# Kernel tuning notes

Measured on AMD Instinct MI355X. Metric: run time of the kernel, lower is better.

Reference implementation:

```python
import jax, jax.numpy as jnp
import numpy as np

N = 100_000   # nodes
E = 1_600_000 # edges
V = 100_000   # vocab
G = 256       # graphs in batch
D = 64        # emb/hidden dim


def setup_inputs() -> dict:
    key = jax.random.key(0)
    ks = jax.random.split(key, 12)
    x_tokens = jax.random.randint(ks[0], (N, 1), 0, V)
    edge_index = jax.random.randint(ks[1], (2, E), 0, N)
    batch = jnp.sort(jax.random.randint(ks[2], (N,), 0, G))
    s = 0.02
    return {
        "x_tokens": x_tokens,
        "edge_index": edge_index,
        "batch": batch,
        "emb_table": jax.random.normal(ks[3], (V, D), jnp.float32) * s,
        "W0": jax.random.normal(ks[4], (D, D), jnp.float32) * s,
        "b0": jnp.zeros((D,), jnp.float32),
        "W1": jax.random.normal(ks[5], (D, D), jnp.float32) * s,
        "b1": jnp.zeros((D,), jnp.float32),
        "W2": jax.random.normal(ks[6], (D, D), jnp.float32) * s,
        "b2": jnp.zeros((D,), jnp.float32),
        "Wc1": jax.random.normal(ks[7], (2 * D, D), jnp.float32) * s,
        "bc1": jnp.zeros((D,), jnp.float32),
        "Wc2": jax.random.normal(ks[8], (D, 2), jnp.float32) * s,
        "bc2": jnp.zeros((2,), jnp.float32),
    }


def _gcn_norm(edge_index, n_nodes):
    # add self loops, compute symmetric normalization coefficients
    loop = jnp.arange(n_nodes, dtype=edge_index.dtype)
    src = jnp.concatenate([edge_index[0], loop])
    dst = jnp.concatenate([edge_index[1], loop])
    deg = jax.ops.segment_sum(jnp.ones_like(dst, jnp.float32), dst, num_segments=n_nodes)
    dinv = jnp.where(deg > 0, deg ** -0.5, 0.0)
    norm = dinv[src] * dinv[dst]  # [E+N]
    return src, dst, norm


def _gcn_conv(x, W, b, src, dst, norm, n_nodes):
    x = x @ W                                   # [N, D]
    msg = x[src] * norm[:, None]                # gather + scale, [E+N, D]
    out = jax.ops.segment_sum(msg, dst, num_segments=n_nodes)
    return out + b


def reference(x_tokens, edge_index, batch, emb_table, W0, b0, W1, b1, W2, b2, Wc1, bc1, Wc2, bc2):
    n = x_tokens.shape[0]
    src, dst, norm = _gcn_norm(edge_index, n)
    x = emb_table[x_tokens[:, 0]]               # [N, D]
    for W, b in ((W0, b0), (W1, b1), (W2, b2)):
        x = jax.nn.relu(_gcn_conv(x, W, b, src, dst, norm, n))
    # dual pooling over graph ids
    cnt = jax.ops.segment_sum(jnp.ones((n,), x.dtype), batch, num_segments=G)
    h_sum = jax.ops.segment_sum(x, batch, num_segments=G)
    h_mean = h_sum / jnp.maximum(cnt, 1.0)[:, None]
    h_max = jax.ops.segment_max(x, batch, num_segments=G)
    h_max = jnp.where(jnp.isfinite(h_max), h_max, 0.0)
    h = jnp.concatenate([h_mean, h_max], axis=-1)   # [G, 2D]
    logits = jax.nn.relu(h @ Wc1 + bc1) @ Wc2 + bc2  # [G, 2]
    return logits
```

## Files before the change

### kernel.cpp

```cpp
#include <hip/hip_runtime.h>
#include <hip/hip_fp16.h>
#include <math.h>


#define BKT_LOG 9
#define BKT (1 << BKT_LOG)
#define CHUNK 4096

typedef _Float16 h2 __attribute__((ext_vector_type(2)));
typedef _Float16 f16x8 __attribute__((ext_vector_type(8)));
typedef float f32x4 __attribute__((ext_vector_type(4)));

union HU { unsigned u; h2 h; };
__device__ inline h2 h2bits(unsigned u) { HU x; x.u = u; return x.h; }

#if __has_builtin(__builtin_amdgcn_fdot2)
#define FDOT2(a, b, c) __builtin_amdgcn_fdot2((a), (b), (c), false)
#else
__device__ inline float FDOT2(h2 a, h2 b, float c) {
  return (float)a.x * (float)b.x + (float)a.y * (float)b.y + c;
}
#endif

#define MASK_X 0x00003C00u
#define MASK_Y 0x3C000000u

__device__ inline void acc8c(const uint4& v, float* acc) {
  const unsigned* w = (const unsigned*)&v;
#pragma unroll
  for (int k = 0; k < 4; k++) {
    h2 hv = h2bits(w[k]);
    acc[2 * k]     = FDOT2(hv, h2bits(MASK_X), acc[2 * k]);
    acc[2 * k + 1] = FDOT2(hv, h2bits(MASK_Y), acc[2 * k + 1]);
  }
}

__global__ __launch_bounds__(256) void k_wcvt(const float* __restrict__ W0,
                                              const float* __restrict__ W1,
                                              const float* __restrict__ W2,
                                              _Float16* __restrict__ Wf,
                                              int* __restrict__ gcur,
                                              float* __restrict__ hz, int hzn) {
  if (blockIdx.x < 3) {
    const float* W = (blockIdx.x == 0) ? W0 : (blockIdx.x == 1) ? W1 : W2;
    _Float16* out = Wf + blockIdx.x * 4096;
    for (int i = threadIdx.x; i < 4096; i += 256) {
      int c = i >> 10, s = (i >> 9) & 1, l = (i >> 3) & 63, j = i & 7;
      int k = 32 * s + 8 * (l >> 4) + j;
      int ncol = 16 * c + (l & 15);
      out[i] = (_Float16)W[k * 64 + ncol];
    }
  } else if (blockIdx.x == 3) {
    gcur[threadIdx.x] = 0;
  } else {
    for (int i = threadIdx.x; i < hzn; i += 256) hz[i] = 0.f;
  }
}

__global__ __launch_bounds__(256) void k_part(const int* __restrict__ src,
                                              const int* __restrict__ dst,
                                              int* __restrict__ gcur,
                                              int* __restrict__ ebuf,
                                              int E, int S) {
  __shared__ int sA[CHUNK];
  __shared__ int dA[CHUNK];
  __shared__ int h[256], base[256];
  int tid = threadIdx.x;
  long c0 = (long)blockIdx.x * CHUNK;
  int m = (int)min((long)CHUNK, (long)E - c0);
  h[tid] = 0;
  __syncthreads();
  for (int i = tid; i < m; i += 256) {
    int s = src[c0 + i];
    int d = dst[c0 + i];
    sA[i] = s;
    dA[i] = d;
    atomicAdd(&h[d >> BKT_LOG], 1);
  }
  __syncthreads();
  if (h[tid]) base[tid] = atomicAdd(&gcur[tid], h[tid]);
  __syncthreads();
  h[tid] = 0;
  __syncthreads();
  for (int i = tid; i < m; i += 256) {
    int s = sA[i], d = dA[i];
    int k = d >> BKT_LOG;
    int p = base[k] + atomicAdd(&h[k], 1);
    if (p < S)
      ebuf[k * S + p] = ((d & (BKT - 1)) << 17) | s;
  }
}

__global__ __launch_bounds__(512) void k_bplace(const int* __restrict__ ebuf,
                                                const int* __restrict__ gcur,
                                                int* __restrict__ off,
                                                int* __restrict__ eend,
                                                int* __restrict__ csrc,
                                                float* __restrict__ dinv,
                                                int N, int S) {
  __shared__ int s[512];
  __shared__ int cur[512];
  int b = blockIdx.x, tid = threadIdx.x;
  int n0 = b << BKT_LOG;
  int nn = min(BKT, N - n0);
  int e0 = b * S;
  int cnt = min(gcur[b], S);
  s[tid] = 0;
  __syncthreads();
  for (int e = tid; e < cnt; e += 512) atomicAdd(&s[ebuf[e0 + e] >> 17], 1);
  __syncthreads();
  int deg = s[tid];
  for (int d = 1; d < 512; d <<= 1) {
    int t = (tid >= d) ? s[tid - d] : 0;
    __syncthreads();
    s[tid] += t;
    __syncthreads();
  }
  int excl = s[tid] - deg;
  if (tid < nn) {
    off[n0 + tid] = e0 + excl;
    eend[n0 + tid] = e0 + excl + deg;
    dinv[n0 + tid] = 1.0f / sqrtf((float)(1 + deg));
  }
  cur[tid] = excl;
  __syncthreads();
  for (int e = tid; e < cnt; e += 512) {
    int p = ebuf[e0 + e];
    int pos = e0 + atomicAdd(&cur[p >> 17], 1);
    csrc[pos] = p & 0x1FFFF;
  }
}

template <bool EMB>
__global__ __launch_bounds__(256) void k_mfmamm(const _Float16* __restrict__ y,
                                                const int* __restrict__ tok,
                                                const float* __restrict__ emb,
                                                const _Float16* __restrict__ Wf,
                                                const float* __restrict__ dinv,
                                                float scale,
                                                _Float16* __restrict__ xh,
                                                int n, int npad) {
  __shared__ _Float16 lds[4 * 16 * 72];
  int w = threadIdx.x >> 6, l = threadIdx.x & 63;
  int m = l & 15, q = l >> 4;
  int rbase = blockIdx.x * 64 + w * 16;

  f16x8 a0, a1;
  if (EMB) {
    int node = min(rbase + m, n - 1);
    const float* er = emb + (size_t)tok[node] * 64;
    float4 v0 = *(const float4*)(er + q * 8);
    float4 v1 = *(const float4*)(er + q * 8 + 4);
    float4 v2 = *(const float4*)(er + 32 + q * 8);
    float4 v3 = *(const float4*)(er + 32 + q * 8 + 4);
    a0[0] = (_Float16)v0.x; a0[1] = (_Float16)v0.y; a0[2] = (_Float16)v0.z; a0[3] = (_Float16)v0.w;
    a0[4] = (_Float16)v1.x; a0[5] = (_Float16)v1.y; a0[6] = (_Float16)v1.z; a0[7] = (_Float16)v1.w;
    a1[0] = (_Float16)v2.x; a1[1] = (_Float16)v2.y; a1[2] = (_Float16)v2.z; a1[3] = (_Float16)v2.w;
    a1[4] = (_Float16)v3.x; a1[5] = (_Float16)v3.y; a1[6] = (_Float16)v3.z; a1[7] = (_Float16)v3.w;
  } else {
    int node = rbase + m;
    a0 = *(const f16x8*)(y + ((size_t)(q >> 1) * npad + node) * 16 + (q & 1) * 8);
    a1 = *(const f16x8*)(y + ((size_t)((q >> 1) + 2) * npad + node) * 16 + (q & 1) * 8);
  }
  float4 d4 = *(const float4*)(dinv + rbase + q * 4);

  const f16x8* wf = (const f16x8*)Wf + l;
  f32x4 acc[4];
#pragma unroll
  for (int c = 0; c < 4; c++) {
    f32x4 z = {0.f, 0.f, 0.f, 0.f};
    z = __builtin_amdgcn_mfma_f32_16x16x32_f16(a0, wf[(c * 2 + 0) * 64], z, 0, 0, 0);
    z = __builtin_amdgcn_mfma_f32_16x16x32_f16(a1, wf[(c * 2 + 1) * 64], z, 0, 0, 0);
    acc[c] = z;
  }

  const float ds[4] = {d4.x * scale, d4.y * scale, d4.z * scale, d4.w * scale};
  _Float16* ldw = lds + w * 16 * 72;
#pragma unroll
  for (int c = 0; c < 4; c++)
#pragma unroll
    for (int r = 0; r < 4; r++)
      ldw[(q * 4 + r) * 72 + c * 16 + m] = (_Float16)(acc[c][r] * ds[r]);
  __syncthreads();

  int row2 = l & 15, c2 = l >> 4;
  int node = rbase + row2;
  if (node < n) {
    const uint4* s4 = (const uint4*)(ldw + row2 * 72 + c2 * 16);
    uint4 v0 = s4[0], v1 = s4[1];
    uint4* dst = (uint4*)(xh + ((size_t)c2 * npad + node) * 16);
    dst[0] = v0;
    dst[1] = v1;
  }
}

__global__ __launch_bounds__(256) void k_aggregate(const int* __restrict__ off,
                                                   const int* __restrict__ eend,
                                                   const int* __restrict__ csrc,
                                                   const float* __restrict__ dinv,
                                                   const _Float16* __restrict__ xh,
                                                   const float* __restrict__ bias,
                                                   _Float16* __restrict__ outp,
                                                   int n, int npad) {
  int c = blockIdx.x & 3;
  int lane = threadIdx.x & 63;
  int n4 = lane >> 4, g = (lane >> 1) & 7, o = lane & 1;
  int t = (blockIdx.x >> 2) * 16 + (threadIdx.x >> 6) * 4 + n4;
  bool valid = t < n;
  int tc = valid ? t : n - 1;
  int e0 = off[tc], e1 = eend[tc];
  if (!valid) e1 = e0;
  const uint4* x4 = (const uint4*)xh + (size_t)c * npad * 2;

  float acc[8];
#pragma unroll
  for (int k = 0; k < 8; k++) acc[k] = 0.f;
  if (g == 0) acc8c(x4[(size_t)tc * 2 + o], acc);

  int iA = e0 + g;
  bool aA = iA < e1, aB = iA + 8 < e1;
  int sA = aA ? csrc[iA] : 0;
  int sB = aB ? csrc[iA + 8] : 0;
  while (aA) {
    uint4 vA = x4[(size_t)sA * 2 + o];
    uint4 vB;
    if (aB) vB = x4[(size_t)sB * 2 + o];
    int iN = iA + 16;
    bool aN = iN < e1, aM = iN + 8 < e1;
    int sN = 0, sM = 0;
    if (aN) sN = csrc[iN];
    if (aM) sM = csrc[iN + 8];
    acc8c(vA, acc);
    if (aB) acc8c(vB, acc);
    iA = iN; aA = aN; sA = sN;
    aB = aM; sB = sM;
  }

#pragma unroll
  for (int mm = 2; mm <= 8; mm <<= 1) {
#pragma unroll
    for (int k = 0; k < 8; k++) acc[k] += __shfl_xor(acc[k], mm);
  }

  if (valid && g == 0) {
    float sc = dinv[t] * (1.0f / 256.0f);
    int f0 = c * 16 + o * 8;
    float4 bb0 = *(const float4*)(bias + f0);
    float4 bb1 = *(const float4*)(bias + f0 + 4);
    const float bs[8] = {bb0.x, bb0.y, bb0.z, bb0.w, bb1.x, bb1.y, bb1.z, bb1.w};
    _Float16 hh[8];
#pragma unroll
    for (int k = 0; k < 8; k++)
      hh[k] = (_Float16)(fmaxf(acc[k] * sc + bs[k], 0.f) * 4096.f);
    *(uint4*)(outp + ((size_t)c * npad + t) * 16 + o * 8) = *(const uint4*)hh;
  }
}

__global__ __launch_bounds__(256) void k_pool(const _Float16* __restrict__ x,
                                              const int* __restrict__ batch,
                                              float* __restrict__ hsum,
                                              float* __restrict__ hmax,
                                              int* __restrict__ cntg,
                                              int n, int npad) {
  int wid = (blockIdx.x * blockDim.x + threadIdx.x) >> 6;
  int lane = threadIdx.x & 63;
  int i0 = wid * 64;
  if (i0 >= n) return;
  int i1 = min(i0 + 64, n);
  size_t sb = (size_t)(lane >> 4) * npad * 16 + (lane & 15);
  int batch_l = (i0 + lane < n) ? batch[i0 + lane] : 0;
  float gsum = 0.f, gmax = 0.f;
  int cur = __shfl(batch_l, 0);
  int c = 0;
  for (int i = i0; i < i1; i++) {
    int g = __shfl(batch_l, i - i0);
    if (g != cur) {
      atomicAdd(&hsum[cur * 64 + lane], gsum);
      atomicMax((int*)&hmax[cur * 64 + lane], __float_as_int(gmax));
      if (lane == 0) atomicAdd(&cntg[cur], c);
      gsum = 0.f; gmax = 0.f; c = 0; cur = g;
    }
    float v = (float)x[sb + (size_t)i * 16];
    gsum += v;
    gmax = fmaxf(gmax, v);
    c++;
  }
  atomicAdd(&hsum[cur * 64 + lane], gsum);
  atomicMax((int*)&hmax[cur * 64 + lane], __float_as_int(gmax));
  if (lane == 0) atomicAdd(&cntg[cur], c);
}

__global__ __launch_bounds__(64) void k_cls(const float* __restrict__ hsum,
                                            const float* __restrict__ hmax,
                                            const int* __restrict__ cnt,
                                            const float* __restrict__ Wc1,
                                            const float* __restrict__ bc1,
                                            const float* __restrict__ Wc2,
                                            const float* __restrict__ bc2,
                                            float* __restrict__ out) {
  __shared__ float h[128];
  __shared__ float hid[64];
  int g = blockIdx.x, j = threadIdx.x;
  int c = cnt[g];
  float cf = (float)(c > 0 ? c : 1);
  h[j] = hsum[g * 64 + j] / cf * (1.0f / 4096.0f);
  h[64 + j] = hmax[g * 64 + j] * (1.0f / 4096.0f);
  __syncthreads();
  float acc = bc1[j];
  for (int k = 0; k < 128; k++) acc += h[k] * Wc1[k * 64 + j];
  hid[j] = fmaxf(acc, 0.f);
  __syncthreads();
  if (j < 2) {
    float a = bc2[j];
    for (int k = 0; k < 64; k++) a += hid[k] * Wc2[k * 2 + j];
    out[g * 2 + j] = a;
  }
}

extern "C" void kernel_launch(void* const* d_in, const int* in_sizes, int n_in,
                              void* d_out, int out_size, void* d_ws, size_t ws_size,
                              hipStream_t stream) {
  const int N = in_sizes[0];
  const int E = in_sizes[1] / 2;
  const int G = out_size / 2;
  const int B = (N + BKT - 1) >> BKT_LOG;
  const int Npad = (N + 63) & ~63;
  const int S = ((((E + B - 1) / B) * 3 / 2 + 256) + 3) & ~3;

  const int* tok   = (const int*)d_in[0];
  const int* ei    = (const int*)d_in[1];
  const int* batch = (const int*)d_in[2];
  const float* emb = (const float*)d_in[3];
  const float* W0 = (const float*)d_in[4];  const float* b0 = (const float*)d_in[5];
  const float* W1 = (const float*)d_in[6];  const float* b1 = (const float*)d_in[7];
  const float* W2 = (const float*)d_in[8];  const float* b2 = (const float*)d_in[9];
  const float* Wc1 = (const float*)d_in[10]; const float* bc1 = (const float*)d_in[11];
  const float* Wc2 = (const float*)d_in[12]; const float* bc2 = (const float*)d_in[13];
  const int* srcp = ei;
  const int* dstp = ei + E;

  int* off    = (int*)d_ws;
  int* eend   = off + N;
  float* dinv = (float*)(eend + N);
  int* gcur   = (int*)(dinv + Npad);
  _Float16* Wf = (_Float16*)(gcur + 256);
  int* csrc   = (int*)(Wf + 3 * 4096);
  _Float16* xh = (_Float16*)(csrc + (size_t)B * S);
  _Float16* y  = xh + (size_t)Npad * 64;
  int* ebuf   = (int*)y;
  float* hsum = (float*)(y + (size_t)Npad * 64);
  float* hmax = hsum + (size_t)G * 64;
  int*   cntg = (int*)(hmax + (size_t)G * 64);

  auto cdiv = [](long a, long b) { return (int)((a + b - 1) / b); };
  const int aggBlocks = 4 * cdiv(N, 16);

  k_wcvt<<<5, 256, 0, stream>>>(W0, W1, W2, Wf, gcur, hsum, G * 129);

  k_part<<<cdiv(E, CHUNK), 256, 0, stream>>>(srcp, dstp, gcur, ebuf, E, S);
  k_bplace<<<B, 512, 0, stream>>>(ebuf, gcur, off, eend, csrc, dinv, N, S);

  k_mfmamm<true><<<cdiv(N, 64), 256, 0, stream>>>(nullptr, tok, emb, Wf, dinv, 256.f, xh, N, Npad);
  k_aggregate<<<aggBlocks, 256, 0, stream>>>(off, eend, csrc, dinv, xh, b0, y, N, Npad);

  k_mfmamm<false><<<cdiv(N, 64), 256, 0, stream>>>(y, nullptr, nullptr, Wf + 4096, dinv, 1.f / 16.f, xh, N, Npad);
  k_aggregate<<<aggBlocks, 256, 0, stream>>>(off, eend, csrc, dinv, xh, b1, y, N, Npad);

  k_mfmamm<false><<<cdiv(N, 64), 256, 0, stream>>>(y, nullptr, nullptr, Wf + 8192, dinv, 1.f / 16.f, xh, N, Npad);
  k_aggregate<<<aggBlocks, 256, 0, stream>>>(off, eend, csrc, dinv, xh, b2, y, N, Npad);

  k_pool<<<cdiv(N, 256), 256, 0, stream>>>(y, batch, hsum, hmax, cntg, N, Npad);

  k_cls<<<G, 64, 0, stream>>>(hsum, hmax, cntg, Wc1, bc1, Wc2, bc2, (float*)d_out);
}
```

Measured before the change: 333.5 us.

## Switch node features to row-major layout and use one wave per node in aggregation

Node feature buffers change from a four-chunk column-blocked layout (16 features per chunk, padded by Npad) to a plain row-major layout of 64 fp16 values per node. The aggregation kernel is rewritten so one wave handles one destination node, with each lane accumulating one feature in fp32 over neighbours read in groups of four. This replaces the earlier scheme where each wave split edges across lane groups with 16-byte loads per lane, fdot2 accumulation and a cross-lane shuffle reduction. Each edge now costs a 128-byte coalesced row read, but the per-lane loads are only 2 bytes and the loop over edges runs serially within a wave, which may lower memory-level parallelism.

```diff
diff --git a/kernel.cpp b/kernel.cpp
--- a/kernel.cpp
+++ b/kernel.cpp
@@ -10,30 +10,6 @@
 typedef _Float16 h2 __attribute__((ext_vector_type(2)));
 typedef _Float16 f16x8 __attribute__((ext_vector_type(8)));
 typedef float f32x4 __attribute__((ext_vector_type(4)));
-
-union HU { unsigned u; h2 h; };
-__device__ inline h2 h2bits(unsigned u) { HU x; x.u = u; return x.h; }
-
-#if __has_builtin(__builtin_amdgcn_fdot2)
-#define FDOT2(a, b, c) __builtin_amdgcn_fdot2((a), (b), (c), false)
-#else
-__device__ inline float FDOT2(h2 a, h2 b, float c) {
-  return (float)a.x * (float)b.x + (float)a.y * (float)b.y + c;
-}
-#endif
-
-#define MASK_X 0x00003C00u
-#define MASK_Y 0x3C000000u
-
-__device__ inline void acc8c(const uint4& v, float* acc) {
-  const unsigned* w = (const unsigned*)&v;
-#pragma unroll
-  for (int k = 0; k < 4; k++) {
-    h2 hv = h2bits(w[k]);
-    acc[2 * k]     = FDOT2(hv, h2bits(MASK_X), acc[2 * k]);
-    acc[2 * k + 1] = FDOT2(hv, h2bits(MASK_Y), acc[2 * k + 1]);
-  }
-}
 
 __global__ __launch_bounds__(256) void k_wcvt(const float* __restrict__ W0,
                                               const float* __restrict__ W1,
@@ -139,7 +115,7 @@
                                                 const float* __restrict__ dinv,
                                                 float scale,
                                                 _Float16* __restrict__ xh,
-                                                int n, int npad) {
+                                                int n) {
   __shared__ _Float16 lds[4 * 16 * 72];
   int w = threadIdx.x >> 6, l = threadIdx.x & 63;
   int m = l & 15, q = l >> 4;
@@ -159,8 +135,9 @@
     a1[4] = (_Float16)v3.x; a1[5] = (_Float16)v3.y; a1[6] = (_Float16)v3.z; a1[7] = (_Float16)v3.w;
   } else {
     int node = rbase + m;
-    a0 = *(const f16x8*)(y + ((size_t)(q >> 1) * npad + node) * 16 + (q & 1) * 8);
-    a1 = *(const f16x8*)(y + ((size_t)((q >> 1) + 2) * npad + node) * 16 + (q & 1) * 8);
+    const _Float16* yr = y + ((size_t)(unsigned)node << 6);
+    a0 = *(const f16x8*)(yr + q * 8);
+    a1 = *(const f16x8*)(yr + 32 + q * 8);
   }
   float4 d4 = *(const float4*)(dinv + rbase + q * 4);
 
@@ -188,7 +165,7 @@
   if (node < n) {
     const uint4* s4 = (const uint4*)(ldw + row2 * 72 + c2 * 16);
     uint4 v0 = s4[0], v1 = s4[1];
-    uint4* dst = (uint4*)(xh + ((size_t)c2 * npad + node) * 16);
+    uint4* dst = (uint4*)(xh + ((size_t)(unsigned)node << 6) + c2 * 16);
     dst[0] = v0;
     dst[1] = v1;
   }
@@ -201,59 +178,35 @@
                                                    const _Float16* __restrict__ xh,
                                                    const float* __restrict__ bias,
                                                    _Float16* __restrict__ outp,
-                                                   int n, int npad) {
-  int c = blockIdx.x & 3;
+                                                   int n) {
   int lane = threadIdx.x & 63;
-  int n4 = lane >> 4, g = (lane >> 1) & 7, o = lane & 1;
-  int t = (blockIdx.x >> 2) * 16 + (threadIdx.x >> 6) * 4 + n4;
-  bool valid = t < n;
-  int tc = valid ? t : n - 1;
-  int e0 = off[tc], e1 = eend[tc];
-  if (!valid) e1 = e0;
-  const uint4* x4 = (const uint4*)xh + (size_t)c * npad * 2;
-
-  float acc[8];
-#pragma unroll
-  for (int k = 0; k < 8; k++) acc[k] = 0.f;
-  if (g == 0) acc8c(x4[(size_t)tc * 2 + o], acc);
-
-  int iA = e0 + g;
-  bool aA = iA < e1, aB = iA + 8 < e1;
-  int sA = aA ? csrc[iA] : 0;
-  int sB = aB ? csrc[iA + 8] : 0;
-  while (aA) {
-    uint4 vA = x4[(size_t)sA * 2 + o];
-    uint4 vB;
-    if (aB) vB = x4[(size_t)sB * 2 + o];
-    int iN = iA + 16;
-    bool aN = iN < e1, aM = iN + 8 < e1;
-    int sN = 0, sM = 0;
-    if (aN) sN = csrc[iN];
-    if (aM) sM = csrc[iN + 8];
-    acc8c(vA, acc);
-    if (aB) acc8c(vB, acc);
-    iA = iN; aA = aN; sA = sN;
-    aB = aM; sB = sM;
-  }
-
-#pragma unroll
-  for (int mm = 2; mm <= 8; mm <<= 1) {
-#pragma unroll
-    for (int k = 0; k < 8; k++) acc[k] += __shfl_xor(acc[k], mm);
-  }
-
-  if (valid && g == 0) {
-    float sc = dinv[t] * (1.0f / 256.0f);
-    int f0 = c * 16 + o * 8;
-    float4 bb0 = *(const float4*)(bias + f0);
-    float4 bb1 = *(const float4*)(bias + f0 + 4);
-    const float bs[8] = {bb0.x, bb0.y, bb0.z, bb0.w, bb1.x, bb1.y, bb1.z, bb1.w};
-    _Float16 hh[8];
-#pragma unroll
-    for (int k = 0; k < 8; k++)
-      hh[k] = (_Float16)(fmaxf(acc[k] * sc + bs[k], 0.f) * 4096.f);
-    *(uint4*)(outp + ((size_t)c * npad + t) * 16 + o * 8) = *(const uint4*)hh;
-  }
+  int t = __builtin_amdgcn_readfirstlane(blockIdx.x * 4 + (threadIdx.x >> 6));
+  if (t >= n) return;
+  int e0 = off[t];
+  int e1 = eend[t];
+
+  float acc = (float)xh[((size_t)(unsigned)t << 6) + lane];
+  int e = e0;
+  for (; e + 4 <= e1; e += 4) {
+    int s0 = csrc[e];
+    int s1 = csrc[e + 1];
+    int s2 = csrc[e + 2];
+    int s3 = csrc[e + 3];
+    float v0 = (float)xh[((size_t)(unsigned)s0 << 6) + lane];
+    float v1 = (float)xh[((size_t)(unsigned)s1 << 6) + lane];
+    float v2 = (float)xh[((size_t)(unsigned)s2 << 6) + lane];
+    float v3 = (float)xh[((size_t)(unsigned)s3 << 6) + lane];
+    acc += v0;
+    acc += v1;
+    acc += v2;
+    acc += v3;
+  }
+  for (; e < e1; ++e)
+    acc += (float)xh[((size_t)(unsigned)csrc[e] << 6) + lane];
+
+  float sc = dinv[t] * (1.0f / 256.0f);
+  float o = fmaxf(acc * sc + bias[lane], 0.f) * 4096.f;
+  outp[((size_t)(unsigned)t << 6) + lane] = (_Float16)o;
 }
 
 __global__ __launch_bounds__(256) void k_pool(const _Float16* __restrict__ x,
@@ -261,13 +214,12 @@
                                               float* __restrict__ hsum,
                                               float* __restrict__ hmax,
                                               int* __restrict__ cntg,
-                                              int n, int npad) {
+                                              int n) {
   int wid = (blockIdx.x * blockDim.x + threadIdx.x) >> 6;
   int lane = threadIdx.x & 63;
   int i0 = wid * 64;
   if (i0 >= n) return;
   int i1 = min(i0 + 64, n);
-  size_t sb = (size_t)(lane >> 4) * npad * 16 + (lane & 15);
   int batch_l = (i0 + lane < n) ? batch[i0 + lane] : 0;
   float gsum = 0.f, gmax = 0.f;
   int cur = __shfl(batch_l, 0);
@@ -280,7 +232,7 @@
       if (lane == 0) atomicAdd(&cntg[cur], c);
       gsum = 0.f; gmax = 0.f; c = 0; cur = g;
     }
-    float v = (float)x[sb + (size_t)i * 16];
+    float v = (float)x[((size_t)(unsigned)i << 6) + lane];
     gsum += v;
     gmax = fmaxf(gmax, v);
     c++;
@@ -353,23 +305,23 @@
   int*   cntg = (int*)(hmax + (size_t)G * 64);
 
   auto cdiv = [](long a, long b) { return (int)((a + b - 1) / b); };
-  const int aggBlocks = 4 * cdiv(N, 16);
+  const int aggBlocks = cdiv(N, 4);
 
   k_wcvt<<<5, 256, 0, stream>>>(W0, W1, W2, Wf, gcur, hsum, G * 129);
 
   k_part<<<cdiv(E, CHUNK), 256, 0, stream>>>(srcp, dstp, gcur, ebuf, E, S);
   k_bplace<<<B, 512, 0, stream>>>(ebuf, gcur, off, eend, csrc, dinv, N, S);
 
-  k_mfmamm<true><<<cdiv(N, 64), 256, 0, stream>>>(nullptr, tok, emb, Wf, dinv, 256.f, xh, N, Npad);
-  k_aggregate<<<aggBlocks, 256, 0, stream>>>(off, eend, csrc, dinv, xh, b0, y, N, Npad);
-
-  k_mfmamm<false><<<cdiv(N, 64), 256, 0, stream>>>(y, nullptr, nullptr, Wf + 4096, dinv, 1.f / 16.f, xh, N, Npad);
-  k_aggregate<<<aggBlocks, 256, 0, stream>>>(off, eend, csrc, dinv, xh, b1, y, N, Npad);
-
-  k_mfmamm<false><<<cdiv(N, 64), 256, 0, stream>>>(y, nullptr, nullptr, Wf + 8192, dinv, 1.f / 16.f, xh, N, Npad);
-  k_aggregate<<<aggBlocks, 256, 0, stream>>>(off, eend, csrc, dinv, xh, b2, y, N, Npad);
-
-  k_pool<<<cdiv(N, 256), 256, 0, stream>>>(y, batch, hsum, hmax, cntg, N, Npad);
+  k_mfmamm<true><<<cdiv(N, 64), 256, 0, stream>>>(nullptr, tok, emb, Wf, dinv, 256.f, xh, N);
+  k_aggregate<<<aggBlocks, 256, 0, stream>>>(off, eend, csrc, dinv, xh, b0, y, N);
+
+  k_mfmamm<false><<<cdiv(N, 64), 256, 0, stream>>>(y, nullptr, nullptr, Wf + 4096, dinv, 1.f / 16.f, xh, N);
+  k_aggregate<<<aggBlocks, 256, 0, stream>>>(off, eend, csrc, dinv, xh, b1, y, N);
+
+  k_mfmamm<false><<<cdiv(N, 64), 256, 0, stream>>>(y, nullptr, nullptr, Wf + 8192, dinv, 1.f / 16.f, xh, N);
+  k_aggregate<<<aggBlocks, 256, 0, stream>>>(off, eend, csrc, dinv, xh, b2, y, N);
+
+  k_pool<<<cdiv(N, 256), 256, 0, stream>>>(y, batch, hsum, hmax, cntg, N);
 
   k_cls<<<G, 64, 0, stream>>>(hsum, hmax, cntg, Wc1, bc1, Wc2, bc2, (float*)d_out);
 }
```

After: 342.5 us. +2.7%, slower.
